# Performance work log

Hardware: AMD Instinct MI355X
Metric: run time of the kernel (lower is better)

## Reference

```python
import math
import jax, jax.numpy as jnp
import numpy as np

H = 16  # num_attention_heads
D = 64  # attention_head_size
ALPHA = 32.0  # PB-relax alpha


def setup_inputs() -> dict:
    key = jax.random.key(0)
    ks = jax.random.split(key, 8)
    B, S, C = 4, 1024, 1024
    scale = 1.0 / math.sqrt(C)
    return {
        "hidden_states": jax.random.normal(ks[0], (B, S, C), jnp.float32),
        "attention_mask": jnp.zeros((B, 1, 1, S), jnp.float32),
        "rel_pos": jax.random.normal(ks[1], (B, H, S, S), jnp.float32),
        "rel_2d_pos": jax.random.normal(ks[2], (B, H, S, S), jnp.float32),
        "Wq": jax.random.normal(ks[3], (C, C), jnp.float32) * scale,
        "bq": jnp.zeros((C,), jnp.float32),
        "Wk": jax.random.normal(ks[4], (C, C), jnp.float32) * scale,
        "bk": jnp.zeros((C,), jnp.float32),
        "Wv": jax.random.normal(ks[5], (C, C), jnp.float32) * scale,
        "bv": jnp.zeros((C,), jnp.float32),
    }


def _heads(x, B, S):
    # [B,S,C] -> [B,H,S,D]
    return x.reshape(B, S, H, D).transpose(0, 2, 1, 3)


def cogview_softmax(scores):
    # PB-relax: softmax(((s/alpha) - max(s/alpha)) * alpha)
    s = scores / ALPHA
    m = jnp.max(s, axis=-1, keepdims=True)
    return jax.nn.softmax((s - m) * ALPHA, axis=-1)


def reference(hidden_states, attention_mask, rel_pos, rel_2d_pos,
              Wq, bq, Wk, bk, Wv, bv):
    B, S, C = hidden_states.shape
    inv_sqrt_d = 1.0 / math.sqrt(D)
    # torch nn.Linear: y = x @ W.T + b; here W is stored as [out, in]
    q = _heads(hidden_states @ Wq.T + bq, B, S)  # [B,H,S,D]
    k = _heads(hidden_states @ Wk.T + bk, B, S)
    v = _heads(hidden_states @ Wv.T + bv, B, S)

    scores = jnp.einsum('bhqd,bhkd->bhqk', q * inv_sqrt_d, k)
    scores = scores + (rel_pos + rel_2d_pos) * inv_sqrt_d
    scores = scores + attention_mask  # broadcast [B,1,1,S]

    probs = cogview_softmax(scores)  # dropout prob = 0 (eval)
    ctx = jnp.einsum('bhqk,bhkd->bhqd', probs, v)
    ctx = ctx.transpose(0, 2, 1, 3).reshape(B, S, C)
    return ctx
```

## Files before the change

kernel.cpp:

```cpp
#include <hip/hip_runtime.h>
#include <hip/hip_bf16.h>

typedef __attribute__((ext_vector_type(8))) short bf16x8;
typedef __attribute__((ext_vector_type(4))) float f32x4;

#define LDSG(g, l) __builtin_amdgcn_global_load_lds(                      \
    (const __attribute__((address_space(1))) void*)(g),                   \
    (__attribute__((address_space(3))) void*)(l), 16, 0, 0)

__global__ __launch_bounds__(256) void cvt_kernel(
    const float* __restrict__ hs,
    const float* __restrict__ wq, const float* __restrict__ wk,
    const float* __restrict__ wv,
    __hip_bfloat16* __restrict__ hbf, __hip_bfloat16* __restrict__ wbf)
{
  const int NH = (4 * 1024 * 1024) / 4;
  const int NW = (1024 * 1024) / 4;
  int i = blockIdx.x * 256 + threadIdx.x;
  float4 v;
  __hip_bfloat16* dst;
  if (i < NH) {
    v = ((const float4*)hs)[i];
    dst = hbf + (size_t)i * 4;
  } else {
    int j = i - NH;
    int which = j / NW, r = j - which * NW;
    const float* src = which == 0 ? wq : (which == 1 ? wk : wv);
    v = ((const float4*)src)[r];
    dst = wbf + (size_t)j * 4;
  }
  union { ushort4 u; __hip_bfloat16 b[4]; } o;
  o.b[0] = __float2bfloat16(v.x);
  o.b[1] = __float2bfloat16(v.y);
  o.b[2] = __float2bfloat16(v.z);
  o.b[3] = __float2bfloat16(v.w);
  *((ushort4*)dst) = o.u;
}

__global__ __launch_bounds__(256) void qkv_gemm(
    const __hip_bfloat16* __restrict__ A,
    const __hip_bfloat16* __restrict__ W,
    const float* __restrict__ bq, const float* __restrict__ bk,
    const float* __restrict__ bv,
    __hip_bfloat16* __restrict__ qo, __hip_bfloat16* __restrict__ ko,
    __hip_bfloat16* __restrict__ vo)
{
  const int K = 1024;
  __shared__ __hip_bfloat16 As[128 * 64];
  __shared__ __hip_bfloat16 Bs[128 * 64];
  const int bid = blockIdx.x;
  const int bm = bid & 31, bn = bid >> 5;
  const int m0 = bm * 128, n0 = bn * 128;
  const int tid = threadIdx.x, wid = tid >> 6, lane = tid & 63;
  const int wm = wid >> 1, wn = wid & 1;

  f32x4 acc[4][4] = {};

  const int srow = lane >> 3;
  const int schunk = (lane & 7) ^ srow;

  for (int k0 = 0; k0 < K; k0 += 64) {
#pragma unroll
    for (int p = 0; p < 4; ++p) {
      int r = (wid * 4 + p) * 8 + srow;
      LDSG(&A[(size_t)(m0 + r) * K + k0 + schunk * 8], &As[(wid * 4 + p) * 512]);
      LDSG(&W[(size_t)(n0 + r) * K + k0 + schunk * 8], &Bs[(wid * 4 + p) * 512]);
    }
    __syncthreads();
#pragma unroll
    for (int ks = 0; ks < 2; ++ks) {
      bf16x8 af[4], bfr[4];
#pragma unroll
      for (int mi = 0; mi < 4; ++mi) {
        int row = wm * 64 + mi * 16 + (lane & 15);
        int slot = (ks * 4 + (lane >> 4)) ^ (lane & 7);
        af[mi] = *(const bf16x8*)((const char*)As + row * 128 + slot * 16);
      }
#pragma unroll
      for (int ni = 0; ni < 4; ++ni) {
        int row = wn * 64 + ni * 16 + (lane & 15);
        int slot = (ks * 4 + (lane >> 4)) ^ (lane & 7);
        bfr[ni] = *(const bf16x8*)((const char*)Bs + row * 128 + slot * 16);
      }
#pragma unroll
      for (int mi = 0; mi < 4; ++mi)
#pragma unroll
        for (int ni = 0; ni < 4; ++ni)
          acc[mi][ni] = __builtin_amdgcn_mfma_f32_16x16x32_bf16(
              af[mi], bfr[ni], acc[mi][ni], 0, 0, 0);
    }
    __syncthreads();
  }

#pragma unroll
  for (int ni = 0; ni < 4; ++ni) {
    int n = n0 + wn * 64 + ni * 16 + (lane & 15);
    int which = n >> 10;
    int h = (n >> 6) & 15;
    int d = n & 63;
    const float* bias = which == 0 ? bq : (which == 1 ? bk : bv);
    float bval = bias[n & 1023];
    __hip_bfloat16* dst = which == 0 ? qo : (which == 1 ? ko : vo);
    float scale = (which == 0) ? 0.125f : 1.0f;
#pragma unroll
    for (int mi = 0; mi < 4; ++mi) {
#pragma unroll
      for (int j = 0; j < 4; ++j) {
        int m = m0 + wm * 64 + mi * 16 + (lane >> 4) * 4 + j;
        int b = m >> 10, s = m & 1023;
        float val = (acc[mi][ni][j] + bval) * scale;
        dst[(((size_t)(b * 16 + h) << 10) + s) * 64 + d] = __float2bfloat16(val);
      }
    }
  }
}

__global__ __launch_bounds__(256) void attn_kernel(
    const __hip_bfloat16* __restrict__ q, const __hip_bfloat16* __restrict__ k,
    const __hip_bfloat16* __restrict__ v,
    const float* __restrict__ rel1, const float* __restrict__ rel2,
    const float* __restrict__ mask, float* __restrict__ out)
{
  __shared__ __hip_bfloat16 Ks[64 * 64];
  __shared__ __hip_bfloat16 Vs[64 * 64];
  __shared__ __hip_bfloat16 Ps[4][16 * 64];

  const int bid = blockIdx.x;
  const int bh = bid & 63, qt = bid >> 6;
  const int b = bh >> 4, h = bh & 15;
  const int tid = threadIdx.x, wid = tid >> 6, lane = tid & 63;

  const size_t kvbase = (size_t)bh << 16;

  const int qrow = qt * 64 + wid * 16 + (lane & 15);
  bf16x8 qf[2];
  qf[0] = *(const bf16x8*)&q[kvbase + (size_t)qrow * 64 + (lane >> 4) * 8];
  qf[1] = *(const bf16x8*)&q[kvbase + (size_t)qrow * 64 + 32 + (lane >> 4) * 8];

  f32x4 accO[4] = {};
  float mrun[4], lrun[4];
#pragma unroll
  for (int j = 0; j < 4; ++j) { mrun[j] = -1e30f; lrun[j] = 0.f; }

  const int srow = lane >> 3;
  const int schunk = (lane & 7) ^ srow;
  const float* relp1 = rel1 + ((size_t)bh << 20);
  const float* relp2 = rel2 + ((size_t)bh << 20);
  const int qrow_c = qt * 64 + wid * 16 + (lane >> 4) * 4;

  for (int kt = 0; kt < 16; ++kt) {
    const int kb = kt * 64;

    float r1[4][4], r2[4][4];
#pragma unroll
    for (int ct = 0; ct < 4; ++ct)
#pragma unroll
      for (int j = 0; j < 4; ++j) {
        size_t off = (size_t)(qrow_c + j) * 1024 + kb + ct * 16 + (lane & 15);
        r1[ct][j] = relp1[off];
        r2[ct][j] = relp2[off];
      }

#pragma unroll
    for (int p = 0; p < 2; ++p) {
      int r = (wid * 2 + p) * 8 + srow;
      LDSG(&k[kvbase + (size_t)(kb + r) * 64 + schunk * 8], &Ks[(wid * 2 + p) * 512]);
      LDSG(&v[kvbase + (size_t)(kb + r) * 64 + (lane & 7) * 8], &Vs[(wid * 2 + p) * 512]);
    }
    __syncthreads();

    f32x4 s4[4] = {};
#pragma unroll
    for (int ks = 0; ks < 2; ++ks) {
#pragma unroll
      for (int ct = 0; ct < 4; ++ct) {
        int row = ct * 16 + (lane & 15);
        int slot = (ks * 4 + (lane >> 4)) ^ (lane & 7);
        bf16x8 kf = *(const bf16x8*)((const char*)Ks + row * 128 + slot * 16);
        s4[ct] = __builtin_amdgcn_mfma_f32_16x16x32_bf16(qf[ks], kf, s4[ct], 0, 0, 0);
      }
    }

    float p[4][4], mt[4];
#pragma unroll
    for (int j = 0; j < 4; ++j) mt[j] = -1e30f;
#pragma unroll
    for (int ct = 0; ct < 4; ++ct) {
      float mval = mask[(size_t)b * 1024 + kb + ct * 16 + (lane & 15)];
#pragma unroll
      for (int j = 0; j < 4; ++j) {
        float sv = s4[ct][j] + 0.125f * (r1[ct][j] + r2[ct][j]) + mval;
        p[ct][j] = sv;
        mt[j] = fmaxf(mt[j], sv);
      }
    }
#pragma unroll
    for (int off = 1; off < 16; off <<= 1)
#pragma unroll
      for (int j = 0; j < 4; ++j)
        mt[j] = fmaxf(mt[j], __shfl_xor(mt[j], off, 64));

    float sc[4], lsum[4];
#pragma unroll
    for (int j = 0; j < 4; ++j) {
      float mnew = fmaxf(mrun[j], mt[j]);
      sc[j] = __expf(mrun[j] - mnew);
      mrun[j] = mnew;
      lsum[j] = 0.f;
    }
#pragma unroll
    for (int ct = 0; ct < 4; ++ct)
#pragma unroll
      for (int j = 0; j < 4; ++j) {
        float e = __expf(p[ct][j] - mrun[j]);
        p[ct][j] = e;
        lsum[j] += e;
      }
#pragma unroll
    for (int off = 1; off < 16; off <<= 1)
#pragma unroll
      for (int j = 0; j < 4; ++j) lsum[j] += __shfl_xor(lsum[j], off, 64);
#pragma unroll
    for (int j = 0; j < 4; ++j) lrun[j] = lrun[j] * sc[j] + lsum[j];
#pragma unroll
    for (int dt = 0; dt < 4; ++dt)
#pragma unroll
      for (int j = 0; j < 4; ++j) accO[dt][j] *= sc[j];

    __hip_bfloat16* Pw = &Ps[wid][0];
#pragma unroll
    for (int ct = 0; ct < 4; ++ct)
#pragma unroll
      for (int j = 0; j < 4; ++j)
        Pw[((lane >> 4) * 4 + j) * 64 + ct * 16 + (lane & 15)] =
            __float2bfloat16(p[ct][j]);
    bf16x8 pa[2];
    pa[0] = *(const bf16x8*)&Pw[(lane & 15) * 64 + (lane >> 4) * 8];
    pa[1] = *(const bf16x8*)&Pw[(lane & 15) * 64 + 32 + (lane >> 4) * 8];

#pragma unroll
    for (int ks = 0; ks < 2; ++ks) {
#pragma unroll
      for (int dt = 0; dt < 4; ++dt) {
        bf16x8 vf;
#pragma unroll
        for (int jj = 0; jj < 8; ++jj) {
          int krow = ks * 32 + (lane >> 4) * 8 + jj;
          ((short*)&vf)[jj] =
              *(const short*)&Vs[krow * 64 + dt * 16 + (lane & 15)];
        }
        accO[dt] = __builtin_amdgcn_mfma_f32_16x16x32_bf16(pa[ks], vf, accO[dt], 0, 0, 0);
      }
    }
    __syncthreads();
  }

#pragma unroll
  for (int dt = 0; dt < 4; ++dt)
#pragma unroll
    for (int j = 0; j < 4; ++j) {
      int s = qrow_c + j;
      out[((size_t)(b * 1024 + s)) * 1024 + h * 64 + dt * 16 + (lane & 15)] =
          accO[dt][j] / lrun[j];
    }
}

extern "C" void kernel_launch(void* const* d_in, const int* in_sizes, int n_in,
                              void* d_out, int out_size, void* d_ws,
                              size_t ws_size, hipStream_t stream) {
  const float* hs   = (const float*)d_in[0];
  const float* mask = (const float*)d_in[1];
  const float* rel1 = (const float*)d_in[2];
  const float* rel2 = (const float*)d_in[3];
  const float* Wq   = (const float*)d_in[4];
  const float* bq   = (const float*)d_in[5];
  const float* Wk   = (const float*)d_in[6];
  const float* bk   = (const float*)d_in[7];
  const float* Wv   = (const float*)d_in[8];
  const float* bv   = (const float*)d_in[9];

  char* ws = (char*)d_ws;
  __hip_bfloat16* hbf = (__hip_bfloat16*)(ws);
  __hip_bfloat16* wbf = (__hip_bfloat16*)(ws + 8388608);
  __hip_bfloat16* qb  = (__hip_bfloat16*)(ws + 14680064);
  __hip_bfloat16* kb  = (__hip_bfloat16*)(ws + 23068672);
  __hip_bfloat16* vb  = (__hip_bfloat16*)(ws + 31457280);

  cvt_kernel<<<7168, 256, 0, stream>>>(hs, Wq, Wk, Wv, hbf, wbf);
  qkv_gemm<<<768, 256, 0, stream>>>(hbf, wbf, bq, bk, bv, qb, kb, vb);
  attn_kernel<<<1024, 256, 0, stream>>>(qb, kb, vb, rel1, rel2, mask,
                                        (float*)d_out);
}
```

Baseline: 195.8 us.

## Double-buffer K/V and rel-pos loads, transpose V, use exp2 softmax in attention

The GEMM epilogue now writes V transposed to [B,H,D,S] with vectorized stores, and folds log2(e)/8 into Q so the softmax can use exp2. The attention kernel double-buffers K and V^T tiles in LDS and prefetches the next tile's rel_pos values as float4 into registers while the current tile is computed. It also swaps MFMA operand order so each lane holds a query row, which reduces the row reductions to two shuffles, and uses swizzled vectorized LDS reads for V in place of scalar gathers. The aim is to hide the large rel_pos memory stream and cut LDS and ALU overhead, in exchange for more registers and LDS per block under a 3-blocks-per-SM launch bound.

```diff
diff --git a/kernel.cpp b/kernel.cpp
--- a/kernel.cpp
+++ b/kernel.cpp
@@ -7,6 +7,9 @@
 #define LDSG(g, l) __builtin_amdgcn_global_load_lds(                      \
     (const __attribute__((address_space(1))) void*)(g),                   \
     (__attribute__((address_space(3))) void*)(l), 16, 0, 0)
+
+#define LOG2E 1.44269504088896f
+#define RELSC 0.180336880111112f
 
 __global__ __launch_bounds__(256) void cvt_kernel(
     const float* __restrict__ hs,
@@ -100,169 +103,167 @@
     int d = n & 63;
     const float* bias = which == 0 ? bq : (which == 1 ? bk : bv);
     float bval = bias[n & 1023];
-    __hip_bfloat16* dst = which == 0 ? qo : (which == 1 ? ko : vo);
-    float scale = (which == 0) ? 0.125f : 1.0f;
-#pragma unroll
-    for (int mi = 0; mi < 4; ++mi) {
-#pragma unroll
-      for (int j = 0; j < 4; ++j) {
-        int m = m0 + wm * 64 + mi * 16 + (lane >> 4) * 4 + j;
+    if (which == 2) {
+#pragma unroll
+      for (int mi = 0; mi < 4; ++mi) {
+        int m = m0 + wm * 64 + mi * 16 + (lane >> 4) * 4;
         int b = m >> 10, s = m & 1023;
-        float val = (acc[mi][ni][j] + bval) * scale;
-        dst[(((size_t)(b * 16 + h) << 10) + s) * 64 + d] = __float2bfloat16(val);
+        union { ushort4 u; __hip_bfloat16 bb[4]; } o;
+#pragma unroll
+        for (int j = 0; j < 4; ++j)
+          o.bb[j] = __float2bfloat16(acc[mi][ni][j] + bval);
+        *(ushort4*)&vo[((size_t)((b * 16 + h) * 64 + d) << 10) + s] = o.u;
+      }
+    } else {
+      __hip_bfloat16* dst = which == 0 ? qo : ko;
+      float scale = (which == 0) ? RELSC : 1.0f;
+#pragma unroll
+      for (int mi = 0; mi < 4; ++mi) {
+#pragma unroll
+        for (int j = 0; j < 4; ++j) {
+          int m = m0 + wm * 64 + mi * 16 + (lane >> 4) * 4 + j;
+          int b = m >> 10, s = m & 1023;
+          float val = (acc[mi][ni][j] + bval) * scale;
+          dst[(((size_t)(b * 16 + h) << 10) + s) * 64 + d] = __float2bfloat16(val);
+        }
       }
     }
   }
 }
 
-__global__ __launch_bounds__(256) void attn_kernel(
-    const __hip_bfloat16* __restrict__ q, const __hip_bfloat16* __restrict__ k,
-    const __hip_bfloat16* __restrict__ v,
+__global__ __launch_bounds__(256, 3) void attn_kernel(
+    const __hip_bfloat16* __restrict__ qg, const __hip_bfloat16* __restrict__ kg,
+    const __hip_bfloat16* __restrict__ vtg,
     const float* __restrict__ rel1, const float* __restrict__ rel2,
     const float* __restrict__ mask, float* __restrict__ out)
 {
-  __shared__ __hip_bfloat16 Ks[64 * 64];
-  __shared__ __hip_bfloat16 Vs[64 * 64];
+  __shared__ __hip_bfloat16 Ks[2][64 * 64];
+  __shared__ __hip_bfloat16 Vts[2][64 * 64];
   __shared__ __hip_bfloat16 Ps[4][16 * 64];
 
   const int bid = blockIdx.x;
   const int bh = bid & 63, qt = bid >> 6;
   const int b = bh >> 4, h = bh & 15;
   const int tid = threadIdx.x, wid = tid >> 6, lane = tid & 63;
+  const int lg = lane >> 4, ln15 = lane & 15;
 
   const size_t kvbase = (size_t)bh << 16;
-
-  const int qrow = qt * 64 + wid * 16 + (lane & 15);
+  const int q0 = qt * 64 + wid * 16;
+
   bf16x8 qf[2];
-  qf[0] = *(const bf16x8*)&q[kvbase + (size_t)qrow * 64 + (lane >> 4) * 8];
-  qf[1] = *(const bf16x8*)&q[kvbase + (size_t)qrow * 64 + 32 + (lane >> 4) * 8];
+  qf[0] = *(const bf16x8*)&qg[kvbase + (size_t)(q0 + ln15) * 64 + lg * 8];
+  qf[1] = *(const bf16x8*)&qg[kvbase + (size_t)(q0 + ln15) * 64 + 32 + lg * 8];
 
   f32x4 accO[4] = {};
-  float mrun[4], lrun[4];
-#pragma unroll
-  for (int j = 0; j < 4; ++j) { mrun[j] = -1e30f; lrun[j] = 0.f; }
-
-  const int srow = lane >> 3;
-  const int schunk = (lane & 7) ^ srow;
-  const float* relp1 = rel1 + ((size_t)bh << 20);
-  const float* relp2 = rel2 + ((size_t)bh << 20);
-  const int qrow_c = qt * 64 + wid * 16 + (lane >> 4) * 4;
-
-  for (int kt = 0; kt < 16; ++kt) {
-    const int kb = kt * 64;
-
-    float r1[4][4], r2[4][4];
-#pragma unroll
-    for (int ct = 0; ct < 4; ++ct)
-#pragma unroll
-      for (int j = 0; j < 4; ++j) {
-        size_t off = (size_t)(qrow_c + j) * 1024 + kb + ct * 16 + (lane & 15);
-        r1[ct][j] = relp1[off];
-        r2[ct][j] = relp2[off];
-      }
-
-#pragma unroll
-    for (int p = 0; p < 2; ++p) {
-      int r = (wid * 2 + p) * 8 + srow;
-      LDSG(&k[kvbase + (size_t)(kb + r) * 64 + schunk * 8], &Ks[(wid * 2 + p) * 512]);
-      LDSG(&v[kvbase + (size_t)(kb + r) * 64 + (lane & 7) * 8], &Vs[(wid * 2 + p) * 512]);
-    }
-    __syncthreads();
-
-    f32x4 s4[4] = {};
-#pragma unroll
-    for (int ks = 0; ks < 2; ++ks) {
-#pragma unroll
-      for (int ct = 0; ct < 4; ++ct) {
-        int row = ct * 16 + (lane & 15);
-        int slot = (ks * 4 + (lane >> 4)) ^ (lane & 7);
-        bf16x8 kf = *(const bf16x8*)((const char*)Ks + row * 128 + slot * 16);
-        s4[ct] = __builtin_amdgcn_mfma_f32_16x16x32_bf16(qf[ks], kf, s4[ct], 0, 0, 0);
-      }
-    }
-
-    float p[4][4], mt[4];
-#pragma unroll
-    for (int j = 0; j < 4; ++j) mt[j] = -1e30f;
-#pragma unroll
-    for (int ct = 0; ct < 4; ++ct) {
-      float mval = mask[(size_t)b * 1024 + kb + ct * 16 + (lane & 15)];
-#pragma unroll
-      for (int j = 0; j < 4; ++j) {
-        float sv = s4[ct][j] + 0.125f * (r1[ct][j] + r2[ct][j]) + mval;
-        p[ct][j] = sv;
-        mt[j] = fmaxf(mt[j], sv);
-      }
-    }
-#pragma unroll
-    for (int off = 1; off < 16; off <<= 1)
-#pragma unroll
-      for (int j = 0; j < 4; ++j)
-        mt[j] = fmaxf(mt[j], __shfl_xor(mt[j], off, 64));
-
-    float sc[4], lsum[4];
-#pragma unroll
-    for (int j = 0; j < 4; ++j) {
-      float mnew = fmaxf(mrun[j], mt[j]);
-      sc[j] = __expf(mrun[j] - mnew);
-      mrun[j] = mnew;
-      lsum[j] = 0.f;
-    }
-#pragma unroll
-    for (int ct = 0; ct < 4; ++ct)
-#pragma unroll
-      for (int j = 0; j < 4; ++j) {
-        float e = __expf(p[ct][j] - mrun[j]);
-        p[ct][j] = e;
-        lsum[j] += e;
-      }
-#pragma unroll
-    for (int off = 1; off < 16; off <<= 1)
-#pragma unroll
-      for (int j = 0; j < 4; ++j) lsum[j] += __shfl_xor(lsum[j], off, 64);
-#pragma unroll
-    for (int j = 0; j < 4; ++j) lrun[j] = lrun[j] * sc[j] + lsum[j];
-#pragma unroll
-    for (int dt = 0; dt < 4; ++dt)
-#pragma unroll
-      for (int j = 0; j < 4; ++j) accO[dt][j] *= sc[j];
-
-    __hip_bfloat16* Pw = &Ps[wid][0];
-#pragma unroll
-    for (int ct = 0; ct < 4; ++ct)
-#pragma unroll
-      for (int j = 0; j < 4; ++j)
-        Pw[((lane >> 4) * 4 + j) * 64 + ct * 16 + (lane & 15)] =
-            __float2bfloat16(p[ct][j]);
-    bf16x8 pa[2];
-    pa[0] = *(const bf16x8*)&Pw[(lane & 15) * 64 + (lane >> 4) * 8];
-    pa[1] = *(const bf16x8*)&Pw[(lane & 15) * 64 + 32 + (lane >> 4) * 8];
-
-#pragma unroll
-    for (int ks = 0; ks < 2; ++ks) {
-#pragma unroll
-      for (int dt = 0; dt < 4; ++dt) {
-        bf16x8 vf;
-#pragma unroll
-        for (int jj = 0; jj < 8; ++jj) {
-          int krow = ks * 32 + (lane >> 4) * 8 + jj;
-          ((short*)&vf)[jj] =
-              *(const short*)&Vs[krow * 64 + dt * 16 + (lane & 15)];
-        }
-        accO[dt] = __builtin_amdgcn_mfma_f32_16x16x32_bf16(pa[ks], vf, accO[dt], 0, 0, 0);
-      }
-    }
-    __syncthreads();
-  }
-
-#pragma unroll
-  for (int dt = 0; dt < 4; ++dt)
-#pragma unroll
-    for (int j = 0; j < 4; ++j) {
-      int s = qrow_c + j;
-      out[((size_t)(b * 1024 + s)) * 1024 + h * 64 + dt * 16 + (lane & 15)] =
-          accO[dt][j] / lrun[j];
-    }
+  float mrun = -1e30f, lrun = 0.f;
+
+  const int srow = lane >> 3, sc8 = lane & 7;
+  const float* relp1 = rel1 + ((size_t)bh << 20) + (size_t)(q0 + ln15) * 1024;
+  const float* relp2 = rel2 + ((size_t)bh << 20) + (size_t)(q0 + ln15) * 1024;
+  const float* maskp = mask + ((size_t)b << 10);
+
+  float4 ra[2][2][4];
+
+#define REL_LOAD(BUF, KB) do {                                              \
+    _Pragma("unroll") for (int ct = 0; ct < 4; ++ct) {                      \
+      ra[BUF][0][ct] = *(const float4*)&relp1[(KB) + ct * 16 + lg * 4];     \
+      ra[BUF][1][ct] = *(const float4*)&relp2[(KB) + ct * 16 + lg * 4];     \
+    } } while (0)
+
+#define STAGE(BUF, KB) do {                                                 \
+    _Pragma("unroll") for (int pp = 0; pp < 2; ++pp) {                      \
+      int rr = (wid * 2 + pp) * 8 + srow;                                   \
+      LDSG(&kg[kvbase + (size_t)((KB) + rr) * 64 + (sc8 ^ (rr & 7)) * 8],   \
+           &Ks[BUF][(wid * 2 + pp) * 512]);                                 \
+      LDSG(&vtg[kvbase + (size_t)rr * 1024 + (KB) + (sc8 ^ (rr & 7)) * 8],  \
+           &Vts[BUF][(wid * 2 + pp) * 512]);                                \
+    } } while (0)
+
+#define BODY(CB, KT) do {                                                   \
+    if ((KT) + 1 < 16) {                                                    \
+      REL_LOAD((CB) ^ 1, ((KT) + 1) * 64);                                  \
+      STAGE((CB) ^ 1, ((KT) + 1) * 64);                                     \
+    }                                                                       \
+    f32x4 st[4] = {};                                                       \
+    _Pragma("unroll") for (int ks = 0; ks < 2; ++ks)                        \
+      _Pragma("unroll") for (int ct = 0; ct < 4; ++ct) {                    \
+        int row = ct * 16 + ln15;                                           \
+        bf16x8 kf = *(const bf16x8*)((const char*)&Ks[CB][0] + row * 128 +  \
+                                     (((ks * 4 + lg) ^ (row & 7)) * 16));   \
+        st[ct] = __builtin_amdgcn_mfma_f32_16x16x32_bf16(kf, qf[ks], st[ct],\
+                                                         0, 0, 0);          \
+      }                                                                     \
+    float p[4][4]; float mt = -1e30f;                                       \
+    const int kb_ = (KT) * 64;                                              \
+    _Pragma("unroll") for (int ct = 0; ct < 4; ++ct) {                      \
+      float4 mv = *(const float4*)&maskp[kb_ + ct * 16 + lg * 4];           \
+      _Pragma("unroll") for (int j = 0; j < 4; ++j) {                       \
+        float sv = st[ct][j] +                                              \
+                   RELSC * (((const float*)&ra[CB][0][ct])[j] +             \
+                            ((const float*)&ra[CB][1][ct])[j]) +            \
+                   LOG2E * ((const float*)&mv)[j];                          \
+        p[ct][j] = sv; mt = fmaxf(mt, sv);                                  \
+      }                                                                     \
+    }                                                                       \
+    mt = fmaxf(mt, __shfl_xor(mt, 16, 64));                                 \
+    mt = fmaxf(mt, __shfl_xor(mt, 32, 64));                                 \
+    float mnew = fmaxf(mrun, mt);                                           \
+    float sc_ = __builtin_amdgcn_exp2f(mrun - mnew);                        \
+    mrun = mnew;                                                            \
+    float lsum = 0.f;                                                       \
+    _Pragma("unroll") for (int ct = 0; ct < 4; ++ct)                        \
+      _Pragma("unroll") for (int j = 0; j < 4; ++j) {                       \
+        float e = __builtin_amdgcn_exp2f(p[ct][j] - mnew);                  \
+        p[ct][j] = e; lsum += e;                                            \
+      }                                                                     \
+    lsum += __shfl_xor(lsum, 16, 64);                                       \
+    lsum += __shfl_xor(lsum, 32, 64);                                       \
+    lrun = lrun * sc_ + lsum;                                               \
+    _Pragma("unroll") for (int dt = 0; dt < 4; ++dt) accO[dt] *= sc_;       \
+    __hip_bfloat16* Pw = &Ps[wid][0];                                       \
+    _Pragma("unroll") for (int ct = 0; ct < 4; ++ct) {                      \
+      union { ushort4 u; __hip_bfloat16 bb[4]; } w;                         \
+      _Pragma("unroll") for (int j = 0; j < 4; ++j)                         \
+        w.bb[j] = __float2bfloat16(p[ct][j]);                               \
+      *(ushort4*)((char*)Pw + ln15 * 128 +                                  \
+                  ((ct * 32 + lg * 8) ^ ((ln15 & 7) << 4))) = w.u;          \
+    }                                                                       \
+    bf16x8 pt[2];                                                           \
+    pt[0] = *(const bf16x8*)((const char*)Pw + ln15 * 128 +                 \
+                             ((lg * 16) ^ ((ln15 & 7) << 4)));              \
+    pt[1] = *(const bf16x8*)((const char*)Pw + ln15 * 128 +                 \
+                             ((64 + lg * 16) ^ ((ln15 & 7) << 4)));         \
+    _Pragma("unroll") for (int ks = 0; ks < 2; ++ks)                        \
+      _Pragma("unroll") for (int dt = 0; dt < 4; ++dt) {                    \
+        int drow = dt * 16 + ln15;                                          \
+        bf16x8 vf = *(const bf16x8*)((const char*)&Vts[CB][0] + drow * 128 +\
+                                     (((ks * 4 + lg) ^ (drow & 7)) * 16));  \
+        accO[dt] = __builtin_amdgcn_mfma_f32_16x16x32_bf16(vf, pt[ks],      \
+                                                           accO[dt], 0, 0, 0);\
+      }                                                                     \
+    __syncthreads();                                                        \
+  } while (0)
+
+  REL_LOAD(0, 0);
+  STAGE(0, 0);
+  __syncthreads();
+
+  for (int t = 0; t < 8; ++t) {
+    BODY(0, 2 * t);
+    BODY(1, 2 * t + 1);
+  }
+
+  float rl = 1.0f / lrun;
+#pragma unroll
+  for (int dt = 0; dt < 4; ++dt) {
+    float4 o;
+    o.x = accO[dt][0] * rl;
+    o.y = accO[dt][1] * rl;
+    o.z = accO[dt][2] * rl;
+    o.w = accO[dt][3] * rl;
+    *(float4*)&out[((size_t)(b * 1024 + q0 + ln15)) * 1024 + h * 64 +
+                   dt * 16 + lg * 4] = o;
+  }
 }
 
 extern "C" void kernel_launch(void* const* d_in, const int* in_sizes, int n_in,
@@ -284,10 +285,10 @@
   __hip_bfloat16* wbf = (__hip_bfloat16*)(ws + 8388608);
   __hip_bfloat16* qb  = (__hip_bfloat16*)(ws + 14680064);
   __hip_bfloat16* kb  = (__hip_bfloat16*)(ws + 23068672);
-  __hip_bfloat16* vb  = (__hip_bfloat16*)(ws + 31457280);
+  __hip_bfloat16* vtb = (__hip_bfloat16*)(ws + 31457280);
 
   cvt_kernel<<<7168, 256, 0, stream>>>(hs, Wq, Wk, Wv, hbf, wbf);
-  qkv_gemm<<<768, 256, 0, stream>>>(hbf, wbf, bq, bk, bv, qb, kb, vb);
-  attn_kernel<<<1024, 256, 0, stream>>>(qb, kb, vb, rel1, rel2, mask,
+  qkv_gemm<<<768, 256, 0, stream>>>(hbf, wbf, bq, bk, bv, qb, kb, vtb);
+  attn_kernel<<<1024, 256, 0, stream>>>(qb, kb, vtb, rel1, rel2, mask,
                                         (float*)d_out);
 }
```

Measured after the change: 205.6 us. 1.05x slower.
